# Optimization experiments

Measured on AMD Instinct MI355X. Metric: run time of the kernel, lower is better.

Reference implementation:

```python
import jax, jax.numpy as jnp
import numpy as np

N = 50000      # nodes
E = 800000     # edges (avg degree 16)
D_IN = 369     # input feature dim
D = 128        # output_dim / GGNN hidden
T = 13         # max_edge_types
STEPS = 8      # GRU propagation steps
G = 256        # graphs in batch


def setup_inputs() -> dict:
    key = jax.random.key(0)
    ks = jax.random.split(key, 13)
    s = 0.05
    return {
        "x": jax.random.normal(ks[0], (N, D_IN), jnp.float32),
        "edge_index": jax.random.randint(ks[1], (2, E), 0, N, dtype=jnp.int64),
        "edge_attr": jax.random.randint(ks[2], (E,), 0, T, dtype=jnp.int64),
        "batch": jnp.sort(jax.random.randint(ks[3], (N,), 0, G, dtype=jnp.int64)),
        "lin_w": jax.random.normal(ks[4], (D_IN, D), jnp.float32) * s,
        "lin_b": jax.random.normal(ks[5], (D,), jnp.float32) * s,
        # per-edge-type GatedGraphConv: weight[t, step] is [D, D]
        "ggnn_w": jax.random.normal(ks[6], (T, STEPS, D, D), jnp.float32) * s,
        # per-edge-type GRUCell params (torch layout: [3*D, D] rows = r,z,n)
        "gru_w_ih": jax.random.normal(ks[7], (T, 3 * D, D), jnp.float32) * s,
        "gru_w_hh": jax.random.normal(ks[8], (T, 3 * D, D), jnp.float32) * s,
        "gru_b_ih": jax.random.normal(ks[9], (T, 3 * D), jnp.float32) * s,
        "gru_b_hh": jax.random.normal(ks[10], (T, 3 * D), jnp.float32) * s,
        "cls_w": jax.random.normal(ks[11], (D, 2), jnp.float32) * s,
        "cls_b": jax.random.normal(ks[12], (2,), jnp.float32) * s,
    }


def reference(x, edge_index, edge_attr, batch,
              lin_w, lin_b, ggnn_w, gru_w_ih, gru_w_hh, gru_b_ih, gru_b_hh,
              cls_w, cls_b):
    n_nodes = x.shape[0]
    h0 = x @ lin_w + lin_b                     # [N, D]; dropout omitted (eval)
    src, dst = edge_index[0], edge_index[1]

    messages = jnp.zeros_like(h0)
    for t in range(T):                          # fixed small set of edge types
        emask = (edge_attr == t).astype(h0.dtype)   # [E] select edges of this type
        w_ih, w_hh = gru_w_ih[t], gru_w_hh[t]
        b_ih, b_hh = gru_b_ih[t], gru_b_hh[t]

        def step(h, w):
            # message passing: aggregate (h @ w)[src] at dst over type-t edges
            xw = h @ w                           # [N, D]
            m = jax.ops.segment_sum(xw[src] * emask[:, None], dst,
                                    num_segments=n_nodes)
            # GRUCell(m, h)
            gi = m @ w_ih.T + b_ih               # [N, 3D]
            gh = h @ w_hh.T + b_hh
            ir, iz, i_n = jnp.split(gi, 3, axis=-1)
            hr, hz, h_n = jnp.split(gh, 3, axis=-1)
            r = jax.nn.sigmoid(ir + hr)
            z = jax.nn.sigmoid(iz + hz)
            n = jnp.tanh(i_n + r * h_n)
            return (1.0 - z) * n + z * h, None

        h_t, _ = jax.lax.scan(step, h0, ggnn_w[t])   # 8 steps
        messages = messages + h_t

    # global_mean_pool over graphs
    sums = jax.ops.segment_sum(messages, batch, num_segments=G)   # [G, D]
    counts = jax.ops.segment_sum(jnp.ones((n_nodes,), messages.dtype), batch,
                                 num_segments=G)
    pooled = sums / jnp.maximum(counts, 1.0)[:, None]
    return pooled @ cls_w + cls_b                                 # [G, 2]
```

## Files before the change

### kernel.cpp

```cpp
#include <hip/hip_runtime.h>
#include <hip/hip_bf16.h>
#include <stdint.h>

typedef __attribute__((ext_vector_type(8))) short   short8;
typedef __attribute__((ext_vector_type(8))) __bf16  bf16x8;
typedef __attribute__((ext_vector_type(4))) float   f32x4;

#define DEV __device__ __forceinline__

DEV float bf2f(uint16_t u){ union{uint32_t i; float f;} v; v.i = ((uint32_t)u)<<16; return v.f; }
DEV uint16_t f2bf(float f){
  union{ __hip_bfloat16 b; uint16_t u; } v; v.b = __float2bfloat16(f); return v.u;
}
DEV float sigmf(float x){ return 1.0f/(1.0f + __expf(-x)); }
DEV float tanhx(float x){ float e = __expf(-2.0f*x); return 2.0f/(1.0f+e) - 1.0f; }

DEV bf16x8 as_bf(short8 s){ union{ short8 s; bf16x8 b; } u; u.s = s; return u.b; }
DEV f32x4 mfma16(short8 a, short8 b, f32x4 c){
  return __builtin_amdgcn_mfma_f32_16x16x32_bf16(as_bf(a), as_bf(b), c, 0, 0, 0);
}
DEV f32x4 vzero(){ f32x4 v; v[0]=0.f; v[1]=0.f; v[2]=0.f; v[3]=0.f; return v; }

DEV void gload16(const uint16_t* g, uint16_t* l){
  __builtin_amdgcn_global_load_lds((const __attribute__((address_space(1))) void*)g,
                                   (__attribute__((address_space(3))) void*)l, 16, 0, 0);
}

__global__ void cast_bf16_kernel(const float* __restrict__ in, uint16_t* __restrict__ out, int n){
  int i = blockIdx.x*256 + threadIdx.x;
  if (i < n) out[i] = f2bf(in[i]);
}

__global__ void cast_swz_kernel(const float* __restrict__ in, uint16_t* __restrict__ out, int n){
  int i = blockIdx.x*256 + threadIdx.x;
  if (i < n){
    int k = i & 127, row = i >> 7;
    out[(row<<7) + (((k>>3) ^ (row&15))<<3) + (k&7)] = f2bf(in[i]);
  }
}

__global__ void xpad_kernel(const float* __restrict__ x, uint16_t* __restrict__ xb, int rows){
  int i = blockIdx.x*256 + threadIdx.x;
  if (i < rows*384){
    int r = i/384, c = i - r*384;
    xb[i] = (c < 369) ? f2bf(x[r*369 + c]) : (uint16_t)0;
  }
}

__global__ void lwt_kernel(const float* __restrict__ lw, uint16_t* __restrict__ lwT){
  int i = blockIdx.x*256 + threadIdx.x;
  if (i < 128*384){
    int nn = i/384, k = i - nn*384;
    lwT[i] = (k < 369) ? f2bf(lw[k*128 + nn]) : (uint16_t)0;
  }
}

__global__ void bias4_kernel(const float* __restrict__ bih, const float* __restrict__ bhh,
                             float4* __restrict__ b4, int TT){
  int i = blockIdx.x*256 + threadIdx.x;
  if (i < TT*128){
    int t = i >> 7, c = i & 127;
    const float* A = bih + t*384; const float* B = bhh + t*384;
    b4[i] = make_float4(A[c]+B[c], A[128+c]+B[128+c], A[256+c], B[256+c]);
  }
}

__global__ __launch_bounds__(256,2)
void gemm_bt_kernel(const uint16_t* __restrict__ A, const uint16_t* __restrict__ B,
                    uint16_t* __restrict__ C,
                    int lda, int ldb, int M, int K4,
                    const float* __restrict__ bias, int swz,
                    long sA, long sB, long sC, int divA)
{
  int by = blockIdx.y;
  A += (long)(by/divA)*sA; B += (long)by*sB; C += (long)by*sC;
  int tid = threadIdx.x, lane = tid&63, wave = tid>>6;
  int l15 = lane&15, quad = lane>>4;
  int m0 = blockIdx.x*64 + wave*16;
  f32x4 acc[8];
  #pragma unroll
  for (int nf=0; nf<8; ++nf) acc[nf] = vzero();
  int mrow = min(m0 + l15, M-1);
  const char* arow = (const char*)(A + (long)mrow*lda) + quad*16;
  for (int kk=0; kk<K4; ++kk){
    short8 a = *(const short8*)(arow + kk*64);
    #pragma unroll
    for (int nf=0; nf<8; ++nf){
      const char* brow = (const char*)(B + (long)(nf*16+l15)*ldb) + quad*16;
      short8 b = *(const short8*)(brow + kk*64);
      acc[nf] = mfma16(a, b, acc[nf]);
    }
  }
  #pragma unroll
  for (int nf=0; nf<8; ++nf){
    int col = nf*16 + l15;
    float bb = bias ? bias[col] : 0.0f;
    #pragma unroll
    for (int i=0; i<4; ++i){
      int row = m0 + quad*4 + i;
      if (row < M){
        float v = acc[nf][i] + bb;
        int idx = swz ? (row*128 + (((col>>3)^(row&15))<<3) + (col&7)) : (row*128+col);
        C[idx] = f2bf(v);
      }
    }
  }
}

__global__ void edge_count_kernel(const int* __restrict__ ei, const int* __restrict__ ea,
                                  int* __restrict__ cnt, int E, int n){
  int e = blockIdx.x*256 + threadIdx.x;
  if (e < E){
    int dst = ei[E + e];
    int t = ea[e];
    atomicAdd(&cnt[t*n + dst], 1);
  }
}

__global__ void csr_alloc_kernel(const int* __restrict__ cnt, int* __restrict__ row_start,
                                 int* __restrict__ cursor, int* __restrict__ total, int R){
  __shared__ int wsum[4];
  __shared__ int base;
  int i = blockIdx.x*256 + threadIdx.x;
  int c = (i < R) ? cnt[i] : 0;
  int lane = threadIdx.x & 63, wave = threadIdx.x >> 6;
  int x = c;
  #pragma unroll
  for (int d=1; d<64; d<<=1){ int y = __shfl_up(x, d, 64); if (lane >= d) x += y; }
  if (lane == 63) wsum[wave] = x;
  __syncthreads();
  if (threadIdx.x == 0){
    int s0=wsum[0], s1=wsum[1], s2=wsum[2], s3=wsum[3];
    base = atomicAdd(total, s0+s1+s2+s3);
    wsum[0]=0; wsum[1]=s0; wsum[2]=s0+s1; wsum[3]=s0+s1+s2;
  }
  __syncthreads();
  int st = base + wsum[wave] + (x - c);
  if (i < R){ row_start[i] = st; cursor[i] = st; }
}

__global__ void edge_fill_kernel(const int* __restrict__ ei, const int* __restrict__ ea,
                                 int* __restrict__ cursor, int* __restrict__ csr, int E, int n){
  int e = blockIdx.x*256 + threadIdx.x;
  if (e < E){
    int src = ei[e], dst = ei[E+e], t = ea[e];
    int pos = atomicAdd(&cursor[t*n + dst], 1);
    csr[pos] = src;
  }
}

__global__ __launch_bounds__(512, 4)
void ggnn_fused_kernel(const uint16_t* __restrict__ h_in_b,
                       uint16_t* __restrict__ h_out_b,
                       const uint16_t* __restrict__ W1_b,
                       const uint16_t* __restrict__ W2_b,
                       const float4* __restrict__ bias4_b,
                       const int* __restrict__ row_start_b,
                       const int* __restrict__ row_cnt_b,
                       const int* __restrict__ csr_src,
                       int n, int s, int t_off,
                       long hin_stride, long hstride)
{
  __shared__ __align__(16) uint16_t sB[2][128*128];
  const int t = t_off + blockIdx.y;
  const uint16_t* h_in = h_in_b + (long)blockIdx.y*hin_stride;
  uint16_t*       h_out= h_out_b+ (long)blockIdx.y*hstride;
  const uint16_t* W1s = W1_b + (size_t)(t*8+s)*384*128;
  const uint16_t* W2s = W2_b + (size_t)t*384*128;
  const float4*   b4p = bias4_b + t*128;

  const int tid = threadIdx.x, lane = tid&63, wave = tid>>6;
  const int l15 = lane&15, quad = lane>>4;
  const int rbase = blockIdx.x*128;

  const uint16_t* stp[6] = { W1s, W2s, W2s+2*16384, W1s+2*16384, W1s+16384, W2s+16384 };

  {
    const uint16_t* gp = stp[0] + tid*8;
    uint16_t* lp = &sB[0][tid*8];
    #pragma unroll
    for (int it=0; it<4; ++it) gload16(gp + it*4096, lp + it*4096);
  }

  const int ar = min(rbase + wave*16 + l15, n-1);

  float4 b4[8];
  #pragma unroll
  for (int nf=0; nf<8; ++nf) b4[nf] = b4p[nf*16 + l15];

  float ga[4][8];
  #pragma unroll
  for (int kk=0; kk<4; ++kk)
    #pragma unroll
    for (int j=0; j<8; ++j) ga[kk][j] = 0.f;
  {
    int st = row_start_b[(size_t)t*n + ar];
    int cn = row_cnt_b  [(size_t)t*n + ar];
    for (int e=0; e<cn; ++e){
      int src = csr_src[st + e];
      const short8* hr = (const short8*)(h_in + (long)src*128);
      #pragma unroll
      for (int kk=0; kk<4; ++kk){
        short8 v = hr[kk*4 + quad];
        #pragma unroll
        for (int j=0; j<8; ++j) ga[kk][j] += bf2f((uint16_t)v[j]);
      }
    }
  }
  short8 afr[4];
  #pragma unroll
  for (int kk=0; kk<4; ++kk){
    short8 p;
    #pragma unroll
    for (int j=0; j<8; ++j) p[j] = (short)f2bf(ga[kk][j]);
    afr[kk] = p;
  }

  short8 hfr[4];
  {
    const short8* hrow = (const short8*)(h_in + (long)ar*128);
    #pragma unroll
    for (int kk=0; kk<4; ++kk) hfr[kk] = hrow[kk*4 + quad];
  }

  auto mma = [&](const uint16_t* bufp, f32x4 (&acc)[8], const short8 (&frag)[4]){
    #pragma unroll
    for (int kk=0; kk<4; ++kk){
      const int ch = ((kk*4+quad)^l15)<<4;
      short8 a = frag[kk];
      #pragma unroll
      for (int nf=0; nf<8; ++nf){
        short8 b = *(const short8*)((const char*)bufp + (nf*16+l15)*256 + ch);
        acc[nf] = mfma16(a, b, acc[nf]);
      }
    }
  };

  f32x4 rg[8], nn[8];
  #pragma unroll
  for (int nf=0; nf<8; ++nf){ rg[nf]=vzero(); nn[nf]=vzero(); }

  #pragma unroll
  for (int g=0; g<6; ++g){
    if (g < 5){
      __builtin_amdgcn_sched_barrier(0);
      const uint16_t* gp = stp[g+1] + tid*8;
      uint16_t* lp = &sB[(g+1)&1][tid*8];
      #pragma unroll
      for (int it=0; it<4; ++it) gload16(gp + it*4096, lp + it*4096);
      asm volatile("s_waitcnt vmcnt(4)" ::: "memory");
      __builtin_amdgcn_sched_barrier(0);
    } else {
      asm volatile("s_waitcnt vmcnt(0)" ::: "memory");
    }
    __builtin_amdgcn_s_barrier();

    const uint16_t* bufp = sB[g&1];
    if (g == 0)      mma(bufp, rg, afr);
    else if (g == 1){
      mma(bufp, rg, hfr);
      #pragma unroll
      for (int nf=0; nf<8; ++nf){
        float bs = b4[nf].x;
        #pragma unroll
        for (int i=0; i<4; ++i) rg[nf][i] = sigmf(rg[nf][i] + bs);
      }
    }
    else if (g == 2){
      mma(bufp, nn, hfr);
      #pragma unroll
      for (int nf=0; nf<8; ++nf){
        float bin = b4[nf].z, bhn = b4[nf].w;
        #pragma unroll
        for (int i=0; i<4; ++i)
          nn[nf][i] = bin + rg[nf][i]*(nn[nf][i] + bhn);
        rg[nf] = vzero();
      }
    }
    else if (g == 3){
      mma(bufp, nn, afr);
      #pragma unroll
      for (int nf=0; nf<8; ++nf)
        #pragma unroll
        for (int i=0; i<4; ++i) nn[nf][i] = tanhx(nn[nf][i]);
    }
    else if (g == 4) mma(bufp, rg, afr);
    else             mma(bufp, rg, hfr);

    __builtin_amdgcn_s_barrier();
  }

  #pragma unroll
  for (int nf=0; nf<8; ++nf){
    int col = nf*16 + l15;
    float bs = b4[nf].y;
    #pragma unroll
    for (int i=0; i<4; ++i){
      int row = rbase + wave*16 + quad*4 + i;
      if (row < n){
        float z = sigmf(rg[nf][i] + bs);
        float hv = bf2f(h_in[(long)row*128 + col]);
        float hnew = nn[nf][i] + z*(hv - nn[nf][i]);
        h_out[(long)row*128 + col] = f2bf(hnew);
      }
    }
  }
}

__global__ void reduce_kernel(const uint16_t* __restrict__ hfin, float* __restrict__ messages,
                              long stride, int nt, int accumulate, int total8){
  int i = blockIdx.x*256 + threadIdx.x;
  if (i < total8){
    float acc[8];
    #pragma unroll
    for (int j=0;j<8;++j) acc[j] = 0.f;
    if (accumulate){
      #pragma unroll
      for (int j=0;j<8;++j) acc[j] = messages[(long)i*8 + j];
    }
    for (int t=0; t<nt; ++t){
      short8 v = *(const short8*)(hfin + (long)t*stride + (long)i*8);
      #pragma unroll
      for (int j=0;j<8;++j) acc[j] += bf2f((uint16_t)v[j]);
    }
    #pragma unroll
    for (int j=0;j<8;++j) messages[(long)i*8 + j] = acc[j];
  }
}

__global__ void pool_kernel(const float* __restrict__ messages, const int* __restrict__ batch,
                            float* __restrict__ sums, int* __restrict__ cntg, int n){
  int id = blockIdx.x*256 + threadIdx.x;
  int col = id & 127;
  int nb = (id >> 7) * 8;
  float acc = 0.f; int curg = -1; int ccount = 0;
  for (int j=0; j<8; ++j){
    int node = nb + j;
    if (node < n){
      int g = batch[node];
      if (g != curg){
        if (curg >= 0){
          atomicAdd(&sums[curg*128+col], acc);
          if (col == 0) atomicAdd(&cntg[curg], ccount);
        }
        curg = g; acc = 0.f; ccount = 0;
      }
      acc += messages[(long)node*128 + col];
      ccount++;
    }
  }
  if (curg >= 0){
    atomicAdd(&sums[curg*128+col], acc);
    if (col == 0) atomicAdd(&cntg[curg], ccount);
  }
}

__global__ void classify_kernel(const float* __restrict__ sums, const int* __restrict__ cntg,
                                const float* __restrict__ cls_w, const float* __restrict__ cls_b,
                                float* __restrict__ out, int G){
  int g = threadIdx.x;
  if (g < G){
    float inv = 1.0f / fmaxf((float)cntg[g], 1.0f);
    float o0 = 0.f, o1 = 0.f;
    for (int d=0; d<128; ++d){
      float p = sums[g*128+d]*inv;
      o0 += p*cls_w[d*2];
      o1 += p*cls_w[d*2+1];
    }
    out[g*2]   = o0 + cls_b[0];
    out[g*2+1] = o1 + cls_b[1];
  }
}

extern "C" void kernel_launch(void* const* d_in, const int* in_sizes, int n_in,
                              void* d_out, int out_size, void* d_ws, size_t ws_size,
                              hipStream_t stream)
{
  const float* x      = (const float*)d_in[0];
  const int*   ei     = (const int*)d_in[1];
  const int*   ea     = (const int*)d_in[2];
  const int*   batch  = (const int*)d_in[3];
  const float* lin_w  = (const float*)d_in[4];
  const float* lin_b  = (const float*)d_in[5];
  const float* ggnn_w = (const float*)d_in[6];
  const float* w_ih   = (const float*)d_in[7];
  const float* w_hh   = (const float*)d_in[8];
  const float* b_ih   = (const float*)d_in[9];
  const float* b_hh   = (const float*)d_in[10];
  const float* cls_w  = (const float*)d_in[11];
  const float* cls_b  = (const float*)d_in[12];
  float* out = (float*)d_out;

  const int N = in_sizes[3];
  const int E = in_sizes[2];
  const int T = in_sizes[9] / 384;
  const int G = out_size / 2;
  const int STEPS = 8;

  struct Layout {
    float *messages, *sums; int *cntg, *total;
    int *cnt, *row_start, *csr;
    uint16_t *W2t, *W1t, *h0;
    float4 *bias4;
    uint16_t *hA, *hB;
    int *cursor; uint16_t *xb, *lwT, *gwb, *wihb;
    size_t zero_off, zero_len, end;
  };
  auto make_layout = [&](int nh)->Layout{
    Layout L; char* base = (char*)d_ws; char* p = base;
    auto A = [&](size_t b)->char*{ char* r = p; p += (b + 255) & ~(size_t)255; return r; };
    L.messages  = (float*)A((size_t)N*128*4);
    char* z0 = p;
    L.sums      = (float*)A((size_t)G*128*4);
    L.cntg      = (int*)  A((size_t)G*4);
    L.total     = (int*)  A(256);
    L.zero_off = (size_t)(z0 - base); L.zero_len = (size_t)(p - z0);
    L.cnt       = (int*)  A((size_t)T*N*4);
    L.row_start = (int*)  A((size_t)T*N*4);
    L.csr       = (int*)  A((size_t)E*4);
    L.W2t       = (uint16_t*)A((size_t)T*384*128*2);
    L.W1t       = (uint16_t*)A((size_t)T*8*384*128*2);
    L.h0        = (uint16_t*)A((size_t)N*128*2);
    L.bias4     = (float4*)  A((size_t)T*128*16);
    char* R = p;
    size_t hb  = (size_t)N*128*2;
    size_t hba = ((size_t)nh*hb + 255) & ~(size_t)255;
    L.hA = (uint16_t*)R; L.hB = (uint16_t*)(R + hba);
    size_t hreg = 2*hba;
    char* q = R;
    auto B = [&](size_t b)->char*{ char* r = q; q += (b + 255) & ~(size_t)255; return r; };
    L.cursor = (int*)     B((size_t)T*N*4);
    L.xb     = (uint16_t*)B((size_t)N*384*2);
    L.lwT    = (uint16_t*)B((size_t)128*384*2);
    L.gwb    = (uint16_t*)B((size_t)T*8*128*128*2);
    L.wihb   = (uint16_t*)B((size_t)T*384*128*2);
    size_t preg = (size_t)(q - R);
    L.end = (size_t)(R - base) + (hreg > preg ? hreg : preg);
    return L;
  };
  int nh = 1;
  { int cand[6] = {7, 6, 5, 4, 3, 2};
    for (int i=0; i<6; ++i){
      int c = cand[i] < T ? cand[i] : T;
      if (make_layout(c).end <= ws_size){ nh = c; break; }
    } }
  Layout L = make_layout(nh);

  hipMemsetAsync((char*)d_ws + L.zero_off, 0, L.zero_len, stream);
  hipMemsetAsync(L.cnt, 0, (size_t)T*N*4, stream);

  const int ngw = T*8*128*128, nwih = T*384*128;
  cast_bf16_kernel<<<(ngw+255)/256, 256, 0, stream>>>(ggnn_w, L.gwb, ngw);
  cast_bf16_kernel<<<(nwih+255)/256, 256, 0, stream>>>(w_ih, L.wihb, nwih);
  cast_swz_kernel <<<(nwih+255)/256, 256, 0, stream>>>(w_hh, L.W2t, nwih);
  xpad_kernel<<<((N*384)+255)/256, 256, 0, stream>>>(x, L.xb, N);
  lwt_kernel<<<(128*384+255)/256, 256, 0, stream>>>(lin_w, L.lwT);
  bias4_kernel<<<(T*128+255)/256, 256, 0, stream>>>(b_ih, b_hh, L.bias4, T);

  gemm_bt_kernel<<<dim3(6, T*8), 256, 0, stream>>>(L.wihb, L.gwb, L.W1t, 128, 128, 384, 4,
      nullptr, 1, (long)384*128, (long)128*128, (long)384*128, 8);
  gemm_bt_kernel<<<dim3((N+63)/64, 1), 256, 0, stream>>>(L.xb, L.lwT, L.h0, 384, 384, N, 12,
      lin_b, 0, 0, 0, 0, 1);

  edge_count_kernel<<<(E+255)/256, 256, 0, stream>>>(ei, ea, L.cnt, E, N);
  csr_alloc_kernel <<<(T*N+255)/256, 256, 0, stream>>>(L.cnt, L.row_start, L.cursor, L.total, T*N);
  edge_fill_kernel <<<(E+255)/256, 256, 0, stream>>>(ei, ea, L.cursor, L.csr, E, N);

  const int nblk = (N+127)/128;
  const long hs = (long)N*128;
  const int total8 = N*128/8;
  const int ngroups = (T + nh - 1)/nh;

  uint16_t* hbuf[2] = { L.hA, L.hB };

  for (int gidx=0; gidx<ngroups; ++gidx){
    int t0 = gidx*nh, nt = (T - t0 < nh) ? (T - t0) : nh;
    for (int s=0; s<STEPS; ++s){
      const uint16_t* hin = (s==0) ? L.h0 : hbuf[s&1];
      uint16_t* hout = hbuf[(s+1)&1];
      long hin_stride = (s==0) ? 0 : hs;
      ggnn_fused_kernel<<<dim3(nblk, nt), 512, 0, stream>>>(
          hin, hout, L.W1t, L.W2t, L.bias4,
          L.row_start, L.cnt, L.csr, N, s, t0, hin_stride, hs);
    }
    reduce_kernel<<<(total8+255)/256, 256, 0, stream>>>(L.hA, L.messages, hs, nt,
                                                        (gidx>0) ? 1 : 0, total8);
  }

  pool_kernel<<<((N*128)+2047)/2048, 256, 0, stream>>>(L.messages, batch, L.sums, L.cntg, N);
  classify_kernel<<<1, 256, 0, stream>>>(L.sums, L.cntg, cls_w, cls_b, out, G);
}
```

Baseline: 3.750 ms.

## Coalesce neighbor gather and output store through swizzled LDS staging

Restructures the edge-aggregation gather so 16 threads read one source row contiguously (16 bytes each) and stage the summed bf16 row into a swizzled LDS tile, from which MFMA A fragments are then loaded. The epilogue also routes the old h values and new h outputs through LDS so global stores become full 256-byte row writes instead of scattered 2-byte stores. The intent is to cut uncoalesced global traffic in both the gather and the store. The cost is extra LDS traffic, extra barriers, and reuse of the weight double buffer, which must not overlap a pending weight prefetch.

```diff
diff --git a/kernel.cpp b/kernel.cpp
--- a/kernel.cpp
+++ b/kernel.cpp
@@ -167,7 +167,6 @@
   uint16_t*       h_out= h_out_b+ (long)blockIdx.y*hstride;
   const uint16_t* W1s = W1_b + (size_t)(t*8+s)*384*128;
   const uint16_t* W2s = W2_b + (size_t)t*384*128;
-  const float4*   b4p = bias4_b + t*128;
 
   const int tid = threadIdx.x, lane = tid&63, wave = tid>>6;
   const int l15 = lane&15, quad = lane>>4;
@@ -182,46 +181,50 @@
     for (int it=0; it<4; ++it) gload16(gp + it*4096, lp + it*4096);
   }
 
+  {
+    const int c8 = tid & 15;
+    #pragma unroll
+    for (int pass=0; pass<4; ++pass){
+      int lrow = pass*32 + (tid>>4);
+      int gr = rbase + lrow;
+      float acc[8] = {0,0,0,0,0,0,0,0};
+      if (gr < n){
+        int st = row_start_b[(size_t)t*n + gr];
+        int cn = row_cnt_b  [(size_t)t*n + gr];
+        for (int e=0; e<cn; ++e){
+          int src = csr_src[st + e];
+          short8 v = *(const short8*)(h_in + (long)src*128 + c8*8);
+          #pragma unroll
+          for (int j=0; j<8; ++j) acc[j] += bf2f((uint16_t)v[j]);
+        }
+      }
+      short8 pk;
+      #pragma unroll
+      for (int j=0; j<8; ++j) pk[j] = (short)f2bf(acc[j]);
+      *(short8*)((char*)sB[1] + lrow*256 + (((c8 ^ (lrow&15)))<<4)) = pk;
+    }
+  }
+  __syncthreads();
+
   const int ar = min(rbase + wave*16 + l15, n-1);
-
+  short8 afr[4], hfr[4];
+  {
+    const char* abase = (const char*)sB[1] + (wave*16 + l15)*256;
+    const short8* hrow = (const short8*)(h_in + (long)ar*128);
+    #pragma unroll
+    for (int kk=0; kk<4; ++kk){
+      afr[kk] = *(const short8*)(abase + (((kk*4+quad) ^ l15)<<4));
+      hfr[kk] = hrow[kk*4 + quad];
+    }
+  }
+  asm volatile("s_waitcnt lgkmcnt(0)" ::: "memory");
+  __builtin_amdgcn_sched_barrier(0);
+  __builtin_amdgcn_s_barrier();
+
+  const float4* b4p = bias4_b + t*128;
   float4 b4[8];
   #pragma unroll
   for (int nf=0; nf<8; ++nf) b4[nf] = b4p[nf*16 + l15];
-
-  float ga[4][8];
-  #pragma unroll
-  for (int kk=0; kk<4; ++kk)
-    #pragma unroll
-    for (int j=0; j<8; ++j) ga[kk][j] = 0.f;
-  {
-    int st = row_start_b[(size_t)t*n + ar];
-    int cn = row_cnt_b  [(size_t)t*n + ar];
-    for (int e=0; e<cn; ++e){
-      int src = csr_src[st + e];
-      const short8* hr = (const short8*)(h_in + (long)src*128);
-      #pragma unroll
-      for (int kk=0; kk<4; ++kk){
-        short8 v = hr[kk*4 + quad];
-        #pragma unroll
-        for (int j=0; j<8; ++j) ga[kk][j] += bf2f((uint16_t)v[j]);
-      }
-    }
-  }
-  short8 afr[4];
-  #pragma unroll
-  for (int kk=0; kk<4; ++kk){
-    short8 p;
-    #pragma unroll
-    for (int j=0; j<8; ++j) p[j] = (short)f2bf(ga[kk][j]);
-    afr[kk] = p;
-  }
-
-  short8 hfr[4];
-  {
-    const short8* hrow = (const short8*)(h_in + (long)ar*128);
-    #pragma unroll
-    for (int kk=0; kk<4; ++kk) hfr[kk] = hrow[kk*4 + quad];
-  }
 
   auto mma = [&](const uint16_t* bufp, f32x4 (&acc)[8], const short8 (&frag)[4]){
     #pragma unroll
@@ -290,18 +293,45 @@
     __builtin_amdgcn_s_barrier();
   }
 
+  char* wbase = (char*)sB[1] + wave*4096;
+  {
+    char* hb = wbase + l15*256;
+    #pragma unroll
+    for (int kk=0; kk<4; ++kk)
+      *(short8*)(hb + (((kk*4+quad) ^ l15)<<4)) = hfr[kk];
+  }
+  asm volatile("s_waitcnt lgkmcnt(0)" ::: "memory");
+  __builtin_amdgcn_sched_barrier(0);
+
+  char* obase = (char*)sB[0] + wave*4096;
   #pragma unroll
   for (int nf=0; nf<8; ++nf){
     int col = nf*16 + l15;
+    int chunk = col >> 3, elem = col & 7;
     float bs = b4[nf].y;
     #pragma unroll
     for (int i=0; i<4; ++i){
-      int row = rbase + wave*16 + quad*4 + i;
-      if (row < n){
-        float z = sigmf(rg[nf][i] + bs);
-        float hv = bf2f(h_in[(long)row*128 + col]);
-        float hnew = nn[nf][i] + z*(hv - nn[nf][i]);
-        h_out[(long)row*128 + col] = f2bf(hnew);
+      int row_loc = quad*4 + i;
+      int coff = ((chunk ^ row_loc)<<4) + elem*2;
+      float hv = bf2f(*(const uint16_t*)(wbase + row_loc*256 + coff));
+      float z = sigmf(rg[nf][i] + bs);
+      float hnew = nn[nf][i] + z*(hv - nn[nf][i]);
+      *(uint16_t*)(obase + row_loc*256 + coff) = f2bf(hnew);
+    }
+  }
+  asm volatile("s_waitcnt lgkmcnt(0)" ::: "memory");
+  __builtin_amdgcn_sched_barrier(0);
+  __syncthreads();
+
+  {
+    const int pos = tid & 15;
+    #pragma unroll
+    for (int it=0; it<4; ++it){
+      int lrow = it*32 + (tid>>4);
+      int gr = rbase + lrow;
+      if (gr < n){
+        short8 v = *(const short8*)((char*)sB[0] + (lrow>>4)*4096 + (lrow&15)*256 + (pos<<4));
+        *(short8*)(h_out + (long)gr*128 + ((pos ^ (lrow&15))<<3)) = v;
       }
     }
   }
```

After: 4.122 ms. +9.9%, slower.
